# Optimization experiments

Hardware: AMD Instinct MI355X
Metric: run time of the kernel (lower is better)

## Reference

```python
import jax, jax.numpy as jnp
import numpy as np

B, S, H, E = 4, 4096, 2048, 16
ED = H // 4
LN_EPS = 1e-5
ROUTING_SCALE = 0.01
NEG_INF = -1e9


def setup_inputs() -> dict:
    key = jax.random.key(0)
    ks = jax.random.split(key, 10)
    std = 0.02
    w_std = 1.0 / np.sqrt(H)  # roughly nn.Linear default scale
    return {
        "hidden_states": jax.random.normal(ks[0], (B, S, H), jnp.float32),
        "layer_embeddings": jax.random.normal(ks[1], (E, H), jnp.float32) * std,
        "centrality_embeddings": jax.random.normal(ks[2], (E, H), jnp.float32) * std,
        "spatial_embeddings": jax.random.normal(ks[3], (E + 1, 1), jnp.float32) * std,
        "edge_embeddings": jax.random.normal(ks[4], (E, ED), jnp.float32) * std,
        "ln_gamma": jnp.ones((H,), jnp.float32),
        "ln_beta": jnp.zeros((H,), jnp.float32),
        "Wq": jax.random.normal(ks[5], (H, H), jnp.float32) * w_std,
        "bq": jnp.zeros((H,), jnp.float32),
        "Wk": jax.random.normal(ks[6], (H, H), jnp.float32) * w_std,
        "bk": jnp.zeros((H,), jnp.float32),
        "Wv": jax.random.normal(ks[7], (H, H), jnp.float32) * w_std,
        "bv": jnp.zeros((H,), jnp.float32),
        "current_layer": 0,  # current_depth == 0 path: used_experts = {0}
        "available_mask": jnp.ones((E,), jnp.int32).at[0].set(0),
    }


def _layer_norm(x, g, b):
    mu = jnp.mean(x, axis=-1, keepdims=True)
    var = jnp.mean(jnp.square(x - mu), axis=-1, keepdims=True)
    return (x - mu) * jax.lax.rsqrt(var + LN_EPS) * g + b


def reference(hidden_states, layer_embeddings, centrality_embeddings,
              spatial_embeddings, edge_embeddings, ln_gamma, ln_beta,
              Wq, bq, Wk, bk, Wv, bv, current_layer, available_mask):
    avail = available_mask.astype(jnp.float32)  # [E]

    # --- attention scores over experts ---
    current_embed = layer_embeddings[current_layer]                 # [H]
    normed = _layer_norm(hidden_states, ln_gamma, ln_beta)          # [B,S,H]
    hidden_mean = jnp.mean(normed, axis=1)                          # [B,H]
    query_input = current_embed + hidden_mean                       # [B,H]
    layer_features = layer_embeddings + centrality_embeddings       # [E,H]

    q = query_input @ Wq.T + bq                                     # [B,H]
    k = layer_features @ Wk.T + bk                                  # [E,H]
    # v is computed in the original but never used downstream of scores
    _v = layer_features @ Wv.T + bv                                 # [E,H]

    attention = (q @ k.T) / np.sqrt(H)                              # [B,E]

    # --- spatial bias ---
    idx = jnp.arange(E)
    distances = jnp.abs(idx - current_layer)                        # [E]
    spatial_bias = spatial_embeddings[distances, 0]                 # [E]

    # --- edge bias: vectorized form of the per-expert loop ---
    # sum over i in available, i != current: (edge_emb[i] @ edge_emb.T) / max(dist_i,1)
    ew = edge_embeddings @ edge_embeddings.T                        # [E,E]
    scale = 1.0 / jnp.maximum(distances, 1).astype(jnp.float32)     # [E]
    row_mask = avail * (idx != current_layer).astype(jnp.float32)   # [E]
    edge_bias = jnp.einsum("i,ij->j", row_mask * scale, ew)         # [E]

    scores = attention + spatial_bias + edge_bias                   # [B,E]
    scores = jnp.where(avail > 0, scores, NEG_INF)                  # mask unavailable

    # --- routing loss (KL to uniform-over-available, batchmean) ---
    probs = jax.nn.softmax(scores, axis=-1)                         # [B,E]
    num_avail = jnp.sum(avail)
    t = 1.0 / num_avail                                             # scalar target prob
    probs_safe = jnp.clip(probs, 1e-10)
    kl = jnp.sum(t * (jnp.log(t) - jnp.log(probs_safe))) / B
    routing_loss = kl * ROUTING_SCALE

    next_idx = jnp.argmax(probs[0], axis=-1)
    return routing_loss, probs, next_idx
```

## Files before the change

kernel.cpp:

```cpp
#include <hip/hip_runtime.h>
#include <hip/hip_bf16.h>

#define DEV __device__ __forceinline__

constexpr float INV_SQRT_H = 0.022097086912079608f;

constexpr size_t WS_PART = 0;
constexpr size_t WS_MU   = WS_PART + (size_t)4096 * 2048;
constexpr size_t WS_QI   = WS_MU + 4096;
constexpr size_t WS_Q    = WS_QI + 4 * 2048;
constexpr size_t WS_K    = WS_Q + 4 * 2048;

DEV bool is_bf16_probe(const void* g) {
    return ((const unsigned int*)g)[0] == 0x3F803F80u;
}

template <bool BF16>
DEV void load8(const void* base, size_t idx, float* o) {
    if constexpr (BF16) {
        const unsigned short* p = (const unsigned short*)base + idx;
        uint4 u = *(const uint4*)p;
        o[0] = __uint_as_float(u.x << 16); o[1] = __uint_as_float(u.x & 0xFFFF0000u);
        o[2] = __uint_as_float(u.y << 16); o[3] = __uint_as_float(u.y & 0xFFFF0000u);
        o[4] = __uint_as_float(u.z << 16); o[5] = __uint_as_float(u.z & 0xFFFF0000u);
        o[6] = __uint_as_float(u.w << 16); o[7] = __uint_as_float(u.w & 0xFFFF0000u);
    } else {
        const float* p = (const float*)base + idx;
        float4 a = *(const float4*)p;
        float4 b = *(const float4*)(p + 4);
        o[0] = a.x; o[1] = a.y; o[2] = a.z; o[3] = a.w;
        o[4] = b.x; o[5] = b.y; o[6] = b.z; o[7] = b.w;
    }
}

template <bool BF16>
DEV float ld1(const void* base, size_t idx) {
    if constexpr (BF16) {
        unsigned int v = ((const unsigned short*)base)[idx];
        return __uint_as_float(v << 16);
    } else {
        return ((const float*)base)[idx];
    }
}

template <bool BF16>
DEV void st1(void* base, size_t idx, float v) {
    if constexpr (BF16) {
        ((__hip_bfloat16*)base)[idx] = __float2bfloat16(v);
    } else {
        ((float*)base)[idx] = v;
    }
}

template <bool BF16>
DEV void kA_body(const void* hidden, const void* lemb, const void* cemb,
                 const void* Wk, const void* bk, float* ws) {
    int bid = blockIdx.x;
    int wave = threadIdx.x >> 6, lane = threadIdx.x & 63;

    if (bid < 1024) {
        int b = bid >> 8;
        int chunk = bid & 255;
        int pid = bid * 4 + wave;

        float acc[32];
#pragma unroll
        for (int i = 0; i < 32; ++i) acc[i] = 0.f;
        float accmu = 0.f;

        for (int r = 0; r < 4; ++r) {
            int s = chunk * 16 + wave * 4 + r;
            size_t base = ((size_t)(b * 4096 + s)) * 2048;
            float x[32];
#pragma unroll
            for (int j = 0; j < 4; ++j)
                load8<BF16>(hidden, base + j * 512 + lane * 8, &x[j * 8]);
            float s1 = 0.f, s2 = 0.f;
#pragma unroll
            for (int i = 0; i < 32; ++i) { s1 += x[i]; s2 += x[i] * x[i]; }
#pragma unroll
            for (int off = 1; off < 64; off <<= 1) {
                s1 += __shfl_xor(s1, off);
                s2 += __shfl_xor(s2, off);
            }
            float mu = s1 * (1.f / 2048.f);
            float var = s2 * (1.f / 2048.f) - mu * mu;
            float rsig = rsqrtf(var + 1e-5f);
            accmu += rsig * mu;
#pragma unroll
            for (int i = 0; i < 32; ++i) acc[i] += rsig * x[i];
        }

        float* part = ws + WS_PART + (size_t)pid * 2048;
#pragma unroll
        for (int j = 0; j < 4; ++j) {
            float4 v0 = make_float4(acc[j * 8 + 0], acc[j * 8 + 1], acc[j * 8 + 2], acc[j * 8 + 3]);
            float4 v1 = make_float4(acc[j * 8 + 4], acc[j * 8 + 5], acc[j * 8 + 6], acc[j * 8 + 7]);
            *(float4*)(part + j * 512 + lane * 8 + 0) = v0;
            *(float4*)(part + j * 512 + lane * 8 + 4) = v1;
        }
        if (lane == 0) ws[WS_MU + pid] = accmu;
    } else {
        int h = (bid - 1024) * 4 + wave;
        float acc[16];
#pragma unroll
        for (int e = 0; e < 16; ++e) acc[e] = 0.f;
#pragma unroll
        for (int ci = 0; ci < 4; ++ci) {
            int c0 = ci * 512 + lane * 8;
            float w8[8];
            load8<BF16>(Wk, (size_t)h * 2048 + c0, w8);
#pragma unroll
            for (int e = 0; e < 16; ++e) {
                float l8[8], c8[8];
                load8<BF16>(lemb, (size_t)e * 2048 + c0, l8);
                load8<BF16>(cemb, (size_t)e * 2048 + c0, c8);
#pragma unroll
                for (int j = 0; j < 8; ++j) acc[e] += w8[j] * (l8[j] + c8[j]);
            }
        }
#pragma unroll
        for (int e = 0; e < 16; ++e)
#pragma unroll
            for (int off = 1; off < 64; off <<= 1) acc[e] += __shfl_xor(acc[e], off);
        if (lane == 0) {
            float bias = ld1<BF16>(bk, h);
#pragma unroll
            for (int e = 0; e < 16; ++e) ws[WS_K + (size_t)e * 2048 + h] = acc[e] + bias;
        }
    }
}

__global__ __launch_bounds__(256) void kA(const void* hidden, const void* lemb,
                                          const void* cemb, const void* Wk,
                                          const void* bk, const void* probe, float* ws) {
    if (is_bf16_probe(probe)) kA_body<true>(hidden, lemb, cemb, Wk, bk, ws);
    else kA_body<false>(hidden, lemb, cemb, Wk, bk, ws);
}

template <bool BF16>
DEV void kB_body(float* ws, const void* gamma, const void* beta, const void* lemb,
                 const int* curp) {
    int bid = blockIdx.x, tid = threadIdx.x;
    int b = bid >> 6, cc = bid & 63;
    __shared__ float smu[4];
    __shared__ float comb[8][32];

    float4 mv = *(const float4*)(ws + WS_MU + (size_t)b * 1024 + tid * 4);
    float m = mv.x + mv.y + mv.z + mv.w;
#pragma unroll
    for (int off = 1; off < 64; off <<= 1) m += __shfl_xor(m, off);
    if ((tid & 63) == 0) smu[tid >> 6] = m;

    int col = cc * 32 + (tid & 31);
    int pg = tid >> 5;
    float a = 0.f;
#pragma unroll 4
    for (int p = pg * 128; p < pg * 128 + 128; ++p)
        a += ws[WS_PART + ((size_t)(b * 1024 + p)) * 2048 + col];
    comb[pg][tid & 31] = a;
    __syncthreads();
    if (tid < 32) {
        float accmu = smu[0] + smu[1] + smu[2] + smu[3];
        float tot = comb[0][tid] + comb[1][tid] + comb[2][tid] + comb[3][tid] +
                    comb[4][tid] + comb[5][tid] + comb[6][tid] + comb[7][tid];
        int c = cc * 32 + tid;
        float hm = ld1<BF16>(gamma, c) * (tot - accmu) * (1.f / 4096.f) +
                   ld1<BF16>(beta, c);
        int cur = curp[0];
        ws[WS_QI + b * 2048 + c] = ld1<BF16>(lemb, (size_t)cur * 2048 + c) + hm;
    }
}

__global__ __launch_bounds__(256) void kB(float* ws, const void* gamma, const void* beta,
                                          const void* lemb, const int* curp) {
    if (is_bf16_probe(gamma)) kB_body<true>(ws, gamma, beta, lemb, curp);
    else kB_body<false>(ws, gamma, beta, lemb, curp);
}

template <bool BF16>
DEV void kC_body(float* ws, const void* Wq, const void* bq) {
    int bid = blockIdx.x;
    int wave = threadIdx.x >> 6, lane = threadIdx.x & 63;
    int h = bid * 4 + wave;
    float acc[4];
#pragma unroll
    for (int b = 0; b < 4; ++b) acc[b] = 0.f;
#pragma unroll
    for (int ci = 0; ci < 4; ++ci) {
        int c0 = ci * 512 + lane * 8;
        float w8[8];
        load8<BF16>(Wq, (size_t)h * 2048 + c0, w8);
#pragma unroll
        for (int b = 0; b < 4; ++b) {
            const float* qi = ws + WS_QI + (size_t)b * 2048 + c0;
            float4 u1 = *(const float4*)qi;
            float4 u2 = *(const float4*)(qi + 4);
            acc[b] += w8[0] * u1.x + w8[1] * u1.y + w8[2] * u1.z + w8[3] * u1.w +
                      w8[4] * u2.x + w8[5] * u2.y + w8[6] * u2.z + w8[7] * u2.w;
        }
    }
#pragma unroll
    for (int b = 0; b < 4; ++b)
#pragma unroll
        for (int off = 1; off < 64; off <<= 1) acc[b] += __shfl_xor(acc[b], off);
    if (lane == 0) {
        float bias = ld1<BF16>(bq, h);
#pragma unroll
        for (int b = 0; b < 4; ++b) ws[WS_Q + (size_t)b * 2048 + h] = acc[b] + bias;
    }
}

__global__ __launch_bounds__(256) void kC(float* ws, const void* Wq, const void* bq,
                                          const void* probe) {
    if (is_bf16_probe(probe)) kC_body<true>(ws, Wq, bq);
    else kC_body<false>(ws, Wq, bq);
}

template <bool BF16>
DEV void kD_body(float* ws, const void* spat, const void* edge, const int* curp,
                 const int* availp, void* out) {
    __shared__ float att[64];
    int wave = threadIdx.x >> 6, lane64 = threadIdx.x & 63;
    int b = wave;

    float q[32];
#pragma unroll
    for (int ci = 0; ci < 4; ++ci) {
        const float* qp = ws + WS_Q + (size_t)b * 2048 + ci * 512 + lane64 * 8;
        float4 a = *(const float4*)qp;
        float4 c = *(const float4*)(qp + 4);
        q[ci * 8 + 0] = a.x; q[ci * 8 + 1] = a.y; q[ci * 8 + 2] = a.z; q[ci * 8 + 3] = a.w;
        q[ci * 8 + 4] = c.x; q[ci * 8 + 5] = c.y; q[ci * 8 + 6] = c.z; q[ci * 8 + 7] = c.w;
    }
    for (int e = 0; e < 16; ++e) {
        float acc = 0.f;
#pragma unroll
        for (int ci = 0; ci < 4; ++ci) {
            const float* kp = ws + WS_K + (size_t)e * 2048 + ci * 512 + lane64 * 8;
            float4 x1 = *(const float4*)kp;
            float4 x2 = *(const float4*)(kp + 4);
            acc += q[ci * 8 + 0] * x1.x + q[ci * 8 + 1] * x1.y +
                   q[ci * 8 + 2] * x1.z + q[ci * 8 + 3] * x1.w +
                   q[ci * 8 + 4] * x2.x + q[ci * 8 + 5] * x2.y +
                   q[ci * 8 + 6] * x2.z + q[ci * 8 + 7] * x2.w;
        }
#pragma unroll
        for (int off = 1; off < 64; off <<= 1) acc += __shfl_xor(acc, off);
        if (lane64 == 0) att[b * 16 + e] = acc * INV_SQRT_H;
    }
    __syncthreads();
    if (wave != 0) return;

    int lane = lane64;
    int cur = curp[0];
    int av[16];
    int navail = 0;
#pragma unroll
    for (int i = 0; i < 16; ++i) { av[i] = availp[i]; navail += (av[i] != 0); }

    int d0 = lane * 8;
    float w8[8];
#pragma unroll
    for (int qq = 0; qq < 8; ++qq) w8[qq] = 0.f;
    for (int i = 0; i < 16; ++i) {
        if (av[i] && i != cur) {
            int dist = i > cur ? i - cur : cur - i;
            float coef = 1.f / (float)(dist > 1 ? dist : 1);
            float e8[8];
            load8<BF16>(edge, (size_t)i * 512 + d0, e8);
#pragma unroll
            for (int qq = 0; qq < 8; ++qq) w8[qq] += coef * e8[qq];
        }
    }
    float bias[16];
    for (int j = 0; j < 16; ++j) {
        float e8[8];
        load8<BF16>(edge, (size_t)j * 512 + d0, e8);
        float p = w8[0] * e8[0] + w8[1] * e8[1] + w8[2] * e8[2] + w8[3] * e8[3] +
                  w8[4] * e8[4] + w8[5] * e8[5] + w8[6] * e8[6] + w8[7] * e8[7];
#pragma unroll
        for (int off = 1; off < 64; off <<= 1) p += __shfl_xor(p, off);
        bias[j] = p;
    }

    int e = lane & 15;
    int dist_e = e > cur ? e - cur : cur - e;
    float sp = ld1<BF16>(spat, dist_e);
    float s = att[lane] + sp + bias[e];
    if (!av[e]) s = -1e9f;

    float m = s;
#pragma unroll
    for (int off = 1; off < 16; off <<= 1) m = fmaxf(m, __shfl_xor(m, off));
    float ex = expf(s - m);
    float sum = ex;
#pragma unroll
    for (int off = 1; off < 16; off <<= 1) sum += __shfl_xor(sum, off);
    float p = ex / sum;
    st1<BF16>(out, 1 + lane, p);

    float t = 1.f / (float)navail;
    float term = t * (logf(t) - logf(fmaxf(p, 1e-10f)));
    float tot = term;
#pragma unroll
    for (int off = 1; off < 64; off <<= 1) tot += __shfl_xor(tot, off);
    if (lane == 0) st1<BF16>(out, 0, tot * (0.01f / 4.f));

    float m2 = p;
#pragma unroll
    for (int off = 1; off < 16; off <<= 1) m2 = fmaxf(m2, __shfl_xor(m2, off));
    int cand = (p == m2 && lane < 16) ? e : 1000;
#pragma unroll
    for (int off = 1; off < 16; off <<= 1) cand = min(cand, __shfl_xor(cand, off));
    if (lane == 0) st1<BF16>(out, 65, (float)cand);
}

__global__ __launch_bounds__(256) void kD(float* ws, const void* spat, const void* edge,
                                          const void* probe, const int* curp,
                                          const int* availp, void* out) {
    if (is_bf16_probe(probe)) kD_body<true>(ws, spat, edge, curp, availp, out);
    else kD_body<false>(ws, spat, edge, curp, availp, out);
}

extern "C" void kernel_launch(void* const* d_in, const int* in_sizes, int n_in,
                              void* d_out, int out_size, void* d_ws, size_t ws_size,
                              hipStream_t stream) {
    const void* hidden = d_in[0];
    const void* lemb   = d_in[1];
    const void* cemb   = d_in[2];
    const void* spat   = d_in[3];
    const void* edge   = d_in[4];
    const void* gamma  = d_in[5];
    const void* beta   = d_in[6];
    const void* Wq     = d_in[7];
    const void* bq     = d_in[8];
    const void* Wk     = d_in[9];
    const void* bk     = d_in[10];
    const int* curp    = (const int*)d_in[13];
    const int* availp  = (const int*)d_in[14];
    float* ws = (float*)d_ws;

    kA<<<1536, 256, 0, stream>>>(hidden, lemb, cemb, Wk, bk, gamma, ws);
    kB<<<256, 256, 0, stream>>>(ws, gamma, beta, lemb, curp);
    kC<<<512, 256, 0, stream>>>(ws, Wq, bq, gamma);
    kD<<<1, 256, 0, stream>>>(ws, spat, edge, gamma, curp, availp, d_out);
}
```

Baseline: 306.5 us.

## Split LayerNorm stats and weighted row sum into separate passes

Replaces the fused single-pass kernel with two kernels. The first computes per-row rsigma and rsigma*mu, using 8 threads per row. The second re-reads the hidden states to build weighted column partial sums over 8 rows per wave, which halves the partial-sum workspace and the reduction work in kB. The cost is a second full read of the 128MB hidden tensor plus an extra launch, traded for less partial-sum write and read traffic and less register pressure.

```diff
diff --git a/kernel.cpp b/kernel.cpp
--- a/kernel.cpp
+++ b/kernel.cpp
@@ -5,9 +5,10 @@
 
 constexpr float INV_SQRT_H = 0.022097086912079608f;
 
-constexpr size_t WS_PART = 0;
-constexpr size_t WS_MU   = WS_PART + (size_t)4096 * 2048;
-constexpr size_t WS_QI   = WS_MU + 4096;
+constexpr size_t WS_RSIG = 0;
+constexpr size_t WS_MU   = WS_RSIG + 16384;
+constexpr size_t WS_PART = WS_MU + 16384;
+constexpr size_t WS_QI   = WS_PART + (size_t)2048 * 2048;
 constexpr size_t WS_Q    = WS_QI + 4 * 2048;
 constexpr size_t WS_K    = WS_Q + 4 * 2048;
 
@@ -53,55 +54,39 @@
 }
 
 template <bool BF16>
-DEV void kA_body(const void* hidden, const void* lemb, const void* cemb,
+DEV void k1_body(const void* hidden, const void* lemb, const void* cemb,
                  const void* Wk, const void* bk, float* ws) {
     int bid = blockIdx.x;
     int wave = threadIdx.x >> 6, lane = threadIdx.x & 63;
 
-    if (bid < 1024) {
-        int b = bid >> 8;
-        int chunk = bid & 255;
-        int pid = bid * 4 + wave;
-
-        float acc[32];
-#pragma unroll
-        for (int i = 0; i < 32; ++i) acc[i] = 0.f;
-        float accmu = 0.f;
-
-        for (int r = 0; r < 4; ++r) {
-            int s = chunk * 16 + wave * 4 + r;
-            size_t base = ((size_t)(b * 4096 + s)) * 2048;
-            float x[32];
-#pragma unroll
-            for (int j = 0; j < 4; ++j)
-                load8<BF16>(hidden, base + j * 512 + lane * 8, &x[j * 8]);
-            float s1 = 0.f, s2 = 0.f;
-#pragma unroll
-            for (int i = 0; i < 32; ++i) { s1 += x[i]; s2 += x[i] * x[i]; }
-#pragma unroll
-            for (int off = 1; off < 64; off <<= 1) {
-                s1 += __shfl_xor(s1, off);
-                s2 += __shfl_xor(s2, off);
-            }
+    if (bid < 512) {
+        int t = bid * 256 + threadIdx.x;
+        int row = t >> 3;
+        int oct = t & 7;
+        size_t base = (size_t)row * 2048 + oct * 256;
+
+        float s1 = 0.f, s2 = 0.f;
+#pragma unroll 8
+        for (int ci = 0; ci < 32; ++ci) {
+            float x[8];
+            load8<BF16>(hidden, base + ci * 8, x);
+#pragma unroll
+            for (int j = 0; j < 8; ++j) { s1 += x[j]; s2 += x[j] * x[j]; }
+        }
+#pragma unroll
+        for (int off = 1; off < 8; off <<= 1) {
+            s1 += __shfl_xor(s1, off);
+            s2 += __shfl_xor(s2, off);
+        }
+        if (oct == 0) {
             float mu = s1 * (1.f / 2048.f);
             float var = s2 * (1.f / 2048.f) - mu * mu;
             float rsig = rsqrtf(var + 1e-5f);
-            accmu += rsig * mu;
-#pragma unroll
-            for (int i = 0; i < 32; ++i) acc[i] += rsig * x[i];
-        }
-
-        float* part = ws + WS_PART + (size_t)pid * 2048;
-#pragma unroll
-        for (int j = 0; j < 4; ++j) {
-            float4 v0 = make_float4(acc[j * 8 + 0], acc[j * 8 + 1], acc[j * 8 + 2], acc[j * 8 + 3]);
-            float4 v1 = make_float4(acc[j * 8 + 4], acc[j * 8 + 5], acc[j * 8 + 6], acc[j * 8 + 7]);
-            *(float4*)(part + j * 512 + lane * 8 + 0) = v0;
-            *(float4*)(part + j * 512 + lane * 8 + 4) = v1;
-        }
-        if (lane == 0) ws[WS_MU + pid] = accmu;
+            ws[WS_RSIG + row] = rsig;
+            ws[WS_MU + row] = rsig * mu;
+        }
     } else {
-        int h = (bid - 1024) * 4 + wave;
+        int h = (bid - 512) * 4 + wave;
         float acc[16];
 #pragma unroll
         for (int e = 0; e < 16; ++e) acc[e] = 0.f;
@@ -131,11 +116,48 @@
     }
 }
 
-__global__ __launch_bounds__(256) void kA(const void* hidden, const void* lemb,
+__global__ __launch_bounds__(256) void k1(const void* hidden, const void* lemb,
                                           const void* cemb, const void* Wk,
                                           const void* bk, const void* probe, float* ws) {
-    if (is_bf16_probe(probe)) kA_body<true>(hidden, lemb, cemb, Wk, bk, ws);
-    else kA_body<false>(hidden, lemb, cemb, Wk, bk, ws);
+    if (is_bf16_probe(probe)) k1_body<true>(hidden, lemb, cemb, Wk, bk, ws);
+    else k1_body<false>(hidden, lemb, cemb, Wk, bk, ws);
+}
+
+template <bool BF16>
+DEV void k2_body(const void* hidden, float* ws) {
+    int wave = threadIdx.x >> 6, lane = threadIdx.x & 63;
+    int w = blockIdx.x * 4 + wave;
+    int r0 = w * 8;
+    const float* rsigp = ws + WS_RSIG;
+
+    float acc[32];
+#pragma unroll
+    for (int i = 0; i < 32; ++i) acc[i] = 0.f;
+
+#pragma unroll 2
+    for (int r = 0; r < 8; ++r) {
+        float rs = rsigp[r0 + r];
+        float x[32];
+#pragma unroll
+        for (int j = 0; j < 4; ++j)
+            load8<BF16>(hidden, (size_t)(r0 + r) * 2048 + j * 512 + lane * 8, &x[j * 8]);
+#pragma unroll
+        for (int i = 0; i < 32; ++i) acc[i] += rs * x[i];
+    }
+
+    float* part = ws + WS_PART + (size_t)w * 2048;
+#pragma unroll
+    for (int j = 0; j < 4; ++j) {
+        float4 v0 = make_float4(acc[j * 8 + 0], acc[j * 8 + 1], acc[j * 8 + 2], acc[j * 8 + 3]);
+        float4 v1 = make_float4(acc[j * 8 + 4], acc[j * 8 + 5], acc[j * 8 + 6], acc[j * 8 + 7]);
+        *(float4*)(part + j * 512 + lane * 8 + 0) = v0;
+        *(float4*)(part + j * 512 + lane * 8 + 4) = v1;
+    }
+}
+
+__global__ __launch_bounds__(256) void k2(const void* hidden, const void* probe, float* ws) {
+    if (is_bf16_probe(probe)) k2_body<true>(hidden, ws);
+    else k2_body<false>(hidden, ws);
 }
 
 template <bool BF16>
@@ -146,8 +168,12 @@
     __shared__ float smu[4];
     __shared__ float comb[8][32];
 
-    float4 mv = *(const float4*)(ws + WS_MU + (size_t)b * 1024 + tid * 4);
-    float m = mv.x + mv.y + mv.z + mv.w;
+    float m = 0.f;
+#pragma unroll
+    for (int k = 0; k < 4; ++k) {
+        float4 mv = *(const float4*)(ws + WS_MU + (size_t)b * 4096 + k * 1024 + tid * 4);
+        m += mv.x + mv.y + mv.z + mv.w;
+    }
 #pragma unroll
     for (int off = 1; off < 64; off <<= 1) m += __shfl_xor(m, off);
     if ((tid & 63) == 0) smu[tid >> 6] = m;
@@ -156,8 +182,8 @@
     int pg = tid >> 5;
     float a = 0.f;
 #pragma unroll 4
-    for (int p = pg * 128; p < pg * 128 + 128; ++p)
-        a += ws[WS_PART + ((size_t)(b * 1024 + p)) * 2048 + col];
+    for (int p = pg * 64; p < pg * 64 + 64; ++p)
+        a += ws[WS_PART + ((size_t)(b * 512 + p)) * 2048 + col];
     comb[pg][tid & 31] = a;
     __syncthreads();
     if (tid < 32) {
@@ -341,7 +367,8 @@
     const int* availp  = (const int*)d_in[14];
     float* ws = (float*)d_ws;
 
-    kA<<<1536, 256, 0, stream>>>(hidden, lemb, cemb, Wk, bk, gamma, ws);
+    k1<<<1024, 256, 0, stream>>>(hidden, lemb, cemb, Wk, bk, gamma, ws);
+    k2<<<512, 256, 0, stream>>>(hidden, gamma, ws);
     kB<<<256, 256, 0, stream>>>(ws, gamma, beta, lemb, curp);
     kC<<<512, 256, 0, stream>>>(ws, Wq, bq, gamma);
     kD<<<1, 256, 0, stream>>>(ws, spat, edge, gamma, curp, availp, d_out);
```

Result: slower. 322.0 us (+5.1%).
